# Kernel tuning notes

Measured on AMD Instinct MI355X. Metric: run time of the kernel, lower is better.

## Reference

```python
import jax, jax.numpy as jnp
import numpy as np

D = 768
NH = 12
HD = D // NH
N_MLP = 3072
LN_EPS = 1e-6


def layer_norm(x, g, b, eps=LN_EPS):
    mu = jnp.mean(x, axis=-1, keepdims=True)
    var = jnp.mean(jnp.square(x - mu), axis=-1, keepdims=True)
    return (x - mu) * jax.lax.rsqrt(var + eps) * g + b


def setup_inputs() -> dict:
    key = jax.random.key(0)
    ks = jax.random.split(key, 6)
    x = jax.random.normal(ks[0], (2, 4096, D), dtype=jnp.float32)
    # torch Linear weights are (out, in); init std=0.02, zero bias
    W_qkv = 0.02 * jax.random.normal(ks[1], (3 * D, D), dtype=jnp.float32)
    b_qkv = jnp.zeros((3 * D,), dtype=jnp.float32)
    W_proj = 0.02 * jax.random.normal(ks[2], (D, D), dtype=jnp.float32)
    b_proj = jnp.zeros((D,), dtype=jnp.float32)
    W1 = 0.02 * jax.random.normal(ks[3], (N_MLP, D), dtype=jnp.float32)
    b1 = jnp.zeros((N_MLP,), dtype=jnp.float32)
    W2 = 0.02 * jax.random.normal(ks[4], (D, N_MLP), dtype=jnp.float32)
    b2 = jnp.zeros((D,), dtype=jnp.float32)
    g1 = jnp.ones((D,), dtype=jnp.float32)
    beta1 = jnp.zeros((D,), dtype=jnp.float32)
    g2 = jnp.ones((D,), dtype=jnp.float32)
    beta2 = jnp.zeros((D,), dtype=jnp.float32)
    return dict(x=x, W_qkv=W_qkv, b_qkv=b_qkv, W_proj=W_proj, b_proj=b_proj,
                W1=W1, b1=b1, W2=W2, b2=b2,
                g1=g1, beta1=beta1, g2=g2, beta2=beta2)


def reference(x, W_qkv, b_qkv, W_proj, b_proj, W1, b1, W2, b2, g1, beta1, g2, beta2):
    B, T, d = x.shape
    scale = HD ** (-0.5)
    # --- attention branch (pre-norm) ---
    h = layer_norm(x, g1, beta1)
    qkv = h @ W_qkv.T + b_qkv                      # [B,T,3d]
    qkv = qkv.reshape(B, T, 3, NH, HD)
    q, k, v = qkv[:, :, 0], qkv[:, :, 1], qkv[:, :, 2]  # [B,T,NH,HD]
    logits = jnp.einsum('bthc,bshc->bhts', q, k) * scale
    attn = jax.nn.softmax(logits, axis=-1)
    out = jnp.einsum('bhts,bshc->bthc', attn, v).reshape(B, T, d)
    out = out @ W_proj.T + b_proj
    x = x + out
    # --- MLP branch (pre-norm) ---
    h = layer_norm(x, g2, beta2)
    h = jax.nn.gelu(h @ W1.T + b1, approximate=False)
    h = h @ W2.T + b2
    return x + h
```

## Files before the change

kernel.cpp:

```cpp
#include <hip/hip_runtime.h>
#include <cmath>

typedef __attribute__((ext_vector_type(4))) float f32x4;
typedef __attribute__((ext_vector_type(16))) float f32x16;
typedef __attribute__((ext_vector_type(8))) __bf16 bf16x8;
typedef __attribute__((ext_vector_type(8))) unsigned short u16x8;
typedef __attribute__((ext_vector_type(4))) unsigned short u16x4;
typedef __attribute__((ext_vector_type(2))) unsigned int u32x2;
typedef __attribute__((ext_vector_type(4))) unsigned int u32x4;

#define DEV __device__ __forceinline__

DEV unsigned short f2b(float v) {
  __bf16 b = (__bf16)v;
  return __builtin_bit_cast(unsigned short, b);
}

DEV unsigned int cvtpk(float lo, float hi) {
  unsigned int r;
  asm("v_cvt_pk_bf16_f32 %0, %1, %2" : "=v"(r) : "v"(lo), "v"(hi));
  return r;
}

DEV float exp2a(float x) {
  float r;
  asm("v_exp_f32 %0, %1" : "=v"(r) : "v"(x));
  return r;
}

DEV void swap32(unsigned int& x, unsigned int& y) {
  asm("v_permlane32_swap_b32 %0, %1" : "+v"(x), "+v"(y));
}

DEV u32x2 tr_b16(const unsigned short* p) {
  u32x2 r;
  asm volatile("ds_read_b64_tr_b16 %0, %1"
               : "=v"(r)
               : "v"((unsigned int)(unsigned long long)p)
               : "memory");
  return r;
}

DEV void gll16(const void* g, const void* l) {
  __builtin_amdgcn_global_load_lds(
      (const __attribute__((address_space(1))) unsigned int*)(unsigned long long)g,
      (__attribute__((address_space(3))) unsigned int*)(unsigned int)(unsigned long long)l,
      16, 0, 0);
}

__global__ void k_cvt_bf16(const float* __restrict__ src,
                           unsigned short* __restrict__ dst, int n4) {
  int i = blockIdx.x * blockDim.x + threadIdx.x;
  if (i >= n4) return;
  float4 v = ((const float4*)src)[i];
  u16x4 o = {f2b(v.x), f2b(v.y), f2b(v.z), f2b(v.w)};
  *(u16x4*)(dst + (size_t)i * 4) = o;
}

__global__ void k_ln(const float* __restrict__ x, const float* __restrict__ g,
                     const float* __restrict__ be, unsigned short* __restrict__ out) {
  int row = blockIdx.x;
  int l = threadIdx.x;
  const float* xr = x + (size_t)row * 768;
  float4 v[3];
  float s = 0.f, sq = 0.f;
#pragma unroll
  for (int j = 0; j < 3; ++j) {
    v[j] = ((const float4*)xr)[l + 64 * j];
    s += v[j].x + v[j].y + v[j].z + v[j].w;
    sq += v[j].x * v[j].x + v[j].y * v[j].y + v[j].z * v[j].z + v[j].w * v[j].w;
  }
#pragma unroll
  for (int m = 1; m < 64; m <<= 1) {
    s += __shfl_xor(s, m);
    sq += __shfl_xor(sq, m);
  }
  float mu = s * (1.f / 768.f);
  float var = sq * (1.f / 768.f) - mu * mu;
  float rs = rsqrtf(var + 1e-6f);
  unsigned short* orow = out + (size_t)row * 768;
#pragma unroll
  for (int j = 0; j < 3; ++j) {
    int c4 = l + 64 * j;
    float4 gv = ((const float4*)g)[c4];
    float4 bv = ((const float4*)be)[c4];
    u16x4 o = {f2b((v[j].x - mu) * rs * gv.x + bv.x),
               f2b((v[j].y - mu) * rs * gv.y + bv.y),
               f2b((v[j].z - mu) * rs * gv.z + bv.z),
               f2b((v[j].w - mu) * rs * gv.w + bv.w)};
    *(u16x4*)(orow + c4 * 4) = o;
  }
}

template <int MODE, int BM>
__global__ __launch_bounds__(256) void k_gemm(
    const unsigned short* __restrict__ A, const unsigned short* __restrict__ Bw,
    const float* __restrict__ bias, const float* __restrict__ res,
    void* __restrict__ outp, int N, int K) {
  __shared__ unsigned short As[BM * 32];
  __shared__ unsigned short Bs[128 * 32];
  constexpr int MR = BM / 32;
  constexpr int AI = BM / 64;
  const int tid = threadIdx.x;
  const int w = tid >> 6, l = tid & 63;
  const int wr = w >> 1, wc = w & 1;
  const int lr = l & 15, lg = l >> 4;
  const int nwg = gridDim.x * gridDim.y;
  const int bid = blockIdx.y * gridDim.x + blockIdx.x;
  const int swz = (bid & 7) * (nwg >> 3) + (bid >> 3);
  const int bx = swz % gridDim.x, by = swz / gridDim.x;
  const int brow = by * BM, bcol = bx * 128;
  f32x4 acc[MR][4] = {};
  for (int kt = 0; kt < K; kt += 32) {
    __syncthreads();
#pragma unroll
    for (int i = 0; i < AI; ++i) {
      int c = i * 256 + tid;
      gll16(A + (size_t)(brow + (c >> 2)) * K + kt + (c & 3) * 8,
            (const char*)As + (i * 256 + (w << 6)) * 16);
    }
#pragma unroll
    for (int i = 0; i < 2; ++i) {
      int c = i * 256 + tid;
      gll16(Bw + (size_t)(bcol + (c >> 2)) * K + kt + (c & 3) * 8,
            (const char*)Bs + (i * 256 + (w << 6)) * 16);
    }
    asm volatile("s_waitcnt vmcnt(0)" ::: "memory");
    __syncthreads();
    bf16x8 af[MR], bfr[4];
#pragma unroll
    for (int m = 0; m < MR; ++m)
      af[m] = *(const bf16x8*)&As[(wr * (BM / 2) + m * 16 + lr) * 32 + lg * 8];
#pragma unroll
    for (int n = 0; n < 4; ++n)
      bfr[n] = *(const bf16x8*)&Bs[(wc * 64 + n * 16 + lr) * 32 + lg * 8];
#pragma unroll
    for (int m = 0; m < MR; ++m)
#pragma unroll
      for (int n = 0; n < 4; ++n)
        acc[m][n] = __builtin_amdgcn_mfma_f32_16x16x32_bf16(af[m], bfr[n], acc[m][n], 0, 0, 0);
  }
#pragma unroll
  for (int n = 0; n < 4; ++n) {
    int col = bcol + wc * 64 + n * 16 + lr;
    float bv = bias[col];
#pragma unroll
    for (int m = 0; m < MR; ++m) {
      int row0 = brow + wr * (BM / 2) + m * 16 + lg * 4;
#pragma unroll
      for (int r = 0; r < 4; ++r) {
        size_t idx = (size_t)(row0 + r) * N + col;
        float v = acc[m][n][r] + bv;
        if (MODE == 0) {
          ((unsigned short*)outp)[idx] = f2b(v);
        } else if (MODE == 1) {
          ((float*)outp)[idx] = v + res[idx];
        } else if (MODE == 2) {
          ((unsigned short*)outp)[idx] = f2b(0.5f * v * (1.f + erff(v * 0.70710678f)));
        } else {
          ((float*)outp)[idx] = v + res[idx];
        }
      }
    }
  }
}

__global__ __launch_bounds__(256, 3) void k_attn(const unsigned short* __restrict__ qkv,
                                                 unsigned short* __restrict__ out) {
  __shared__ unsigned short Ks[2][64 * 64];
  __shared__ unsigned short Vs[2][4 * 64 * 16];
  const int tid = threadIdx.x;
  const int w = tid >> 6, l = tid & 63;
  const int lq = l & 31, hi = l >> 5;
  const int p = blockIdx.x;
  const int bid = (p & 7) * 96 + (p >> 3);
  const int bh = bid >> 5, qt = bid & 31;
  const int b = bh / 12, h = bh % 12;
  const size_t base = (size_t)b * 4096 * 2304;
  const int qbase = qt * 128 + w * 32;

  const float SC = 0.18033688f;
  bf16x8 qb[4];
#pragma unroll
  for (int s = 0; s < 4; ++s) {
    u16x8 raw = *(const u16x8*)(qkv + base + (size_t)(qbase + lq) * 2304 + h * 64 +
                                s * 16 + hi * 8);
    u32x4 pk;
#pragma unroll
    for (int d = 0; d < 4; ++d) {
      float f0 = __builtin_bit_cast(float, (unsigned int)raw[2 * d] << 16) * SC;
      float f1 = __builtin_bit_cast(float, (unsigned int)raw[2 * d + 1] << 16) * SC;
      pk[d] = cvtpk(f0, f1);
    }
    qb[s] = __builtin_bit_cast(bf16x8, pk);
  }

  const unsigned short* pK = qkv + base + (size_t)(16 * w + (l >> 3)) * 2304 + 768 +
                             h * 64 + (((l & 7) ^ ((l >> 3) & 7)) << 3);
  const unsigned short* pV =
      qkv + base + (size_t)(l >> 1) * 2304 + 1536 + h * 64 + w * 16 + ((l & 1) << 3);
  const size_t STEP = (size_t)64 * 2304;

  {
    const char* dK = (const char*)&Ks[0][0] + w * 2048;
    const char* dV = (const char*)&Vs[0][0] + w * 2048;
    gll16(pK, dK);
    gll16(pK + 8 * 2304, dK + 1024);
    gll16(pV, dV);
    gll16(pV + 32 * 2304, dV + 1024);
    pK += STEP;
    pV += STEP;
  }

  f32x16 O[2] = {};
  float mrun = -1e30f, lrun = 0.f;

  int it = 0;
  for (int t = 0; t < 64; ++t, it ^= 1) {
    asm volatile("s_waitcnt vmcnt(0)" ::: "memory");
    __syncthreads();
    if (t < 63) {
      const char* dK = (const char*)&Ks[it ^ 1][0] + w * 2048;
      const char* dV = (const char*)&Vs[it ^ 1][0] + w * 2048;
      gll16(pK, dK);
      gll16(pK + 8 * 2304, dK + 1024);
      gll16(pV, dV);
      gll16(pV + 32 * 2304, dV + 1024);
      pK += STEP;
      pV += STEP;
    }

    f32x16 st[2] = {{0}, {0}};
    __builtin_amdgcn_s_setprio(1);
#pragma unroll
    for (int kt = 0; kt < 2; ++kt) {
      int key = kt * 32 + lq;
#pragma unroll
      for (int s = 0; s < 4; ++s) {
        bf16x8 ka =
            *(const bf16x8*)&Ks[it][key * 64 + ((s * 16 + hi * 8) ^ ((key & 7) << 3))];
        st[kt] = __builtin_amdgcn_mfma_f32_32x32x16_bf16(ka, qb[s], st[kt], 0, 0, 0);
      }
    }
    __builtin_amdgcn_s_setprio(0);

    float pmax = st[0][0];
#pragma unroll
    for (int kt = 0; kt < 2; ++kt)
#pragma unroll
      for (int r = (kt == 0 ? 1 : 0); r < 16; ++r) pmax = fmaxf(pmax, st[kt][r]);
    pmax = fmaxf(pmax, __shfl_xor(pmax, 32));
    if (!__all(pmax - mrun <= 11.0f)) {
      float mnew = fmaxf(mrun, pmax);
      float al = exp2a(mrun - mnew);
      lrun *= al;
#pragma unroll
      for (int hb = 0; hb < 2; ++hb)
#pragma unroll
        for (int r = 0; r < 16; ++r) O[hb][r] *= al;
      mrun = mnew;
    }
    float s0 = 0.f;
#pragma unroll
    for (int kt = 0; kt < 2; ++kt)
#pragma unroll
      for (int r = 0; r < 16; ++r) {
        float pv = exp2a(st[kt][r] - mrun);
        st[kt][r] = pv;
        s0 += pv;
      }
    lrun += s0 + __shfl_xor(s0, 32);

    u32x4 pf[4];
#pragma unroll
    for (int kt = 0; kt < 2; ++kt)
#pragma unroll
      for (int h2 = 0; h2 < 2; ++h2) {
        int r0 = h2 * 8;
        unsigned int a0 = cvtpk(st[kt][r0 + 0], st[kt][r0 + 1]);
        unsigned int a1 = cvtpk(st[kt][r0 + 2], st[kt][r0 + 3]);
        unsigned int b0 = cvtpk(st[kt][r0 + 4], st[kt][r0 + 5]);
        unsigned int b1 = cvtpk(st[kt][r0 + 6], st[kt][r0 + 7]);
        swap32(a0, b0);
        swap32(a1, b1);
        pf[kt * 2 + h2] = u32x4{a0, a1, b0, b1};
      }

#pragma unroll
    for (int hb = 0; hb < 2; ++hb) {
      u32x2 vt[4][2];
      const unsigned short* vbase = &Vs[it][(hb * 2 + (lq >> 4)) * 1024 + (lq & 15)];
#pragma unroll
      for (int s = 0; s < 4; ++s)
#pragma unroll
        for (int t2 = 0; t2 < 2; ++t2)
          vt[s][t2] = tr_b16(vbase + ((s * 16 + hi * 8 + t2 * 4) << 4));
      asm volatile("s_waitcnt lgkmcnt(0)" ::: "memory");
      __builtin_amdgcn_sched_barrier(0);
      __builtin_amdgcn_s_setprio(1);
#pragma unroll
      for (int s = 0; s < 4; ++s) {
        u32x4 vv = {vt[s][0].x, vt[s][0].y, vt[s][1].x, vt[s][1].y};
        O[hb] = __builtin_amdgcn_mfma_f32_32x32x16_bf16(
            __builtin_bit_cast(bf16x8, vv), __builtin_bit_cast(bf16x8, pf[s]), O[hb], 0, 0, 0);
      }
      __builtin_amdgcn_s_setprio(0);
    }
  }

  float rl = 1.f / lrun;
  unsigned short* orow = out + (size_t)(b * 4096 + qbase + lq) * 768 + h * 64;
#pragma unroll
  for (int hb = 0; hb < 2; ++hb)
#pragma unroll
    for (int g = 0; g < 4; ++g) {
      unsigned int d0 = cvtpk(O[hb][4 * g + 0] * rl, O[hb][4 * g + 1] * rl);
      unsigned int d1 = cvtpk(O[hb][4 * g + 2] * rl, O[hb][4 * g + 3] * rl);
      *(u32x2*)(orow + hb * 32 + 8 * g + 4 * hi) = u32x2{d0, d1};
    }
}

extern "C" void kernel_launch(void* const* d_in, const int* in_sizes, int n_in,
                              void* d_out, int out_size, void* d_ws, size_t ws_size,
                              hipStream_t stream) {
  const float* x = (const float*)d_in[0];
  const float* Wqkv = (const float*)d_in[1];
  const float* bqkv = (const float*)d_in[2];
  const float* Wproj = (const float*)d_in[3];
  const float* bproj = (const float*)d_in[4];
  const float* W1 = (const float*)d_in[5];
  const float* b1 = (const float*)d_in[6];
  const float* W2 = (const float*)d_in[7];
  const float* b2 = (const float*)d_in[8];
  const float* g1 = (const float*)d_in[9];
  const float* be1 = (const float*)d_in[10];
  const float* g2 = (const float*)d_in[11];
  const float* be2 = (const float*)d_in[12];

  char* ws = (char*)d_ws;
  unsigned short* wqkv = (unsigned short*)(ws + 0);
  unsigned short* wproj = (unsigned short*)(ws + 3538944);
  unsigned short* ww1 = (unsigned short*)(ws + 4718592);
  unsigned short* ww2 = (unsigned short*)(ws + 9437184);
  unsigned short* h1 = (unsigned short*)(ws + 14155776);
  unsigned short* qkvb = (unsigned short*)(ws + 26738688);
  unsigned short* attno = (unsigned short*)(ws + 64487424);
  float* x1 = (float*)(ws + 77070336);
  unsigned short* h2 = (unsigned short*)(ws + 102236160);
  unsigned short* m1 = (unsigned short*)(ws + 114819072);

  k_cvt_bf16<<<1728, 256, 0, stream>>>(Wqkv, wqkv, 442368);
  k_cvt_bf16<<<576, 256, 0, stream>>>(Wproj, wproj, 147456);
  k_cvt_bf16<<<2304, 256, 0, stream>>>(W1, ww1, 589824);
  k_cvt_bf16<<<2304, 256, 0, stream>>>(W2, ww2, 589824);

  k_ln<<<8192, 64, 0, stream>>>(x, g1, be1, h1);
  k_gemm<0, 128><<<dim3(18, 64), 256, 0, stream>>>(h1, wqkv, bqkv, nullptr, qkvb, 2304, 768);
  k_attn<<<768, 256, 0, stream>>>(qkvb, attno);
  k_gemm<1, 64><<<dim3(6, 128), 256, 0, stream>>>(attno, wproj, bproj, x, x1, 768, 768);
  k_ln<<<8192, 64, 0, stream>>>(x1, g2, be2, h2);
  k_gemm<2, 128><<<dim3(24, 64), 256, 0, stream>>>(h2, ww1, b1, nullptr, m1, 3072, 768);
  k_gemm<3, 64><<<dim3(6, 128), 256, 0, stream>>>(m1, ww2, b2, x1, (float*)d_out, 768, 3072);
}
```

Baseline: 374.4 us.

## Split attention KV into two halves with merge kernel; widen GEMM K-tile with swizzled LDS

Attention now splits each query tile's 4096-key range into two 2048-key halves. That doubles the grid to 1536 workgroups and raises the occupancy hint to 4. Partial unnormalised outputs and running max/sum are written to fp32 scratch, reusing the m1 and h1 buffers, and a new merge kernel combines them with rescaling. Separately, the GEMM K-step goes from 32 to 64, with an XOR-swizzled LDS layout to avoid bank conflicts, which halves the barrier and wait count per K. The costs are extra global traffic for the fp32 partials, an extra launch, and larger LDS use per GEMM block.

Result: faster. 365.6 us (-2.3%).

```diff
diff --git a/kernel.cpp b/kernel.cpp
--- a/kernel.cpp
+++ b/kernel.cpp
@@ -97,10 +97,10 @@
     const unsigned short* __restrict__ A, const unsigned short* __restrict__ Bw,
     const float* __restrict__ bias, const float* __restrict__ res,
     void* __restrict__ outp, int N, int K) {
-  __shared__ unsigned short As[BM * 32];
-  __shared__ unsigned short Bs[128 * 32];
+  __shared__ unsigned short As[BM * 64];
+  __shared__ unsigned short Bs[128 * 64];
   constexpr int MR = BM / 32;
-  constexpr int AI = BM / 64;
+  constexpr int AI = BM / 32;
   const int tid = threadIdx.x;
   const int w = tid >> 6, l = tid & 63;
   const int wr = w >> 1, wc = w & 1;
@@ -111,34 +111,47 @@
   const int bx = swz % gridDim.x, by = swz / gridDim.x;
   const int brow = by * BM, bcol = bx * 128;
   f32x4 acc[MR][4] = {};
-  for (int kt = 0; kt < K; kt += 32) {
+  for (int kt = 0; kt < K; kt += 64) {
     __syncthreads();
 #pragma unroll
     for (int i = 0; i < AI; ++i) {
       int c = i * 256 + tid;
-      gll16(A + (size_t)(brow + (c >> 2)) * K + kt + (c & 3) * 8,
+      int row = c >> 3, cg = (c & 7) ^ (row & 7);
+      gll16(A + (size_t)(brow + row) * K + kt + cg * 8,
             (const char*)As + (i * 256 + (w << 6)) * 16);
     }
 #pragma unroll
-    for (int i = 0; i < 2; ++i) {
+    for (int i = 0; i < 4; ++i) {
       int c = i * 256 + tid;
-      gll16(Bw + (size_t)(bcol + (c >> 2)) * K + kt + (c & 3) * 8,
+      int row = c >> 3, cg = (c & 7) ^ (row & 7);
+      gll16(Bw + (size_t)(bcol + row) * K + kt + cg * 8,
             (const char*)Bs + (i * 256 + (w << 6)) * 16);
     }
     asm volatile("s_waitcnt vmcnt(0)" ::: "memory");
     __syncthreads();
-    bf16x8 af[MR], bfr[4];
-#pragma unroll
-    for (int m = 0; m < MR; ++m)
-      af[m] = *(const bf16x8*)&As[(wr * (BM / 2) + m * 16 + lr) * 32 + lg * 8];
-#pragma unroll
-    for (int n = 0; n < 4; ++n)
-      bfr[n] = *(const bf16x8*)&Bs[(wc * 64 + n * 16 + lr) * 32 + lg * 8];
-#pragma unroll
-    for (int m = 0; m < MR; ++m)
-#pragma unroll
-      for (int n = 0; n < 4; ++n)
-        acc[m][n] = __builtin_amdgcn_mfma_f32_16x16x32_bf16(af[m], bfr[n], acc[m][n], 0, 0, 0);
+    bf16x8 af[MR][2], bfr[4][2];
+#pragma unroll
+    for (int m = 0; m < MR; ++m) {
+      int row = wr * (BM / 2) + m * 16 + lr;
+#pragma unroll
+      for (int s = 0; s < 2; ++s)
+        af[m][s] = *(const bf16x8*)&As[row * 64 + (((s * 4 + lg) ^ (row & 7)) << 3)];
+    }
+#pragma unroll
+    for (int n = 0; n < 4; ++n) {
+      int row = wc * 64 + n * 16 + lr;
+#pragma unroll
+      for (int s = 0; s < 2; ++s)
+        bfr[n][s] = *(const bf16x8*)&Bs[row * 64 + (((s * 4 + lg) ^ (row & 7)) << 3)];
+    }
+#pragma unroll
+    for (int s = 0; s < 2; ++s)
+#pragma unroll
+      for (int m = 0; m < MR; ++m)
+#pragma unroll
+        for (int n = 0; n < 4; ++n)
+          acc[m][n] =
+              __builtin_amdgcn_mfma_f32_16x16x32_bf16(af[m][s], bfr[n][s], acc[m][n], 0, 0, 0);
   }
 #pragma unroll
   for (int n = 0; n < 4; ++n) {
@@ -165,19 +178,22 @@
   }
 }
 
-__global__ __launch_bounds__(256, 3) void k_attn(const unsigned short* __restrict__ qkv,
-                                                 unsigned short* __restrict__ out) {
+__global__ __launch_bounds__(256, 4) void k_attn(const unsigned short* __restrict__ qkv,
+                                                 f32x4* __restrict__ Opart,
+                                                 float* __restrict__ ml) {
   __shared__ unsigned short Ks[2][64 * 64];
   __shared__ unsigned short Vs[2][4 * 64 * 16];
   const int tid = threadIdx.x;
   const int w = tid >> 6, l = tid & 63;
   const int lq = l & 31, hi = l >> 5;
   const int p = blockIdx.x;
-  const int bid = (p & 7) * 96 + (p >> 3);
-  const int bh = bid >> 5, qt = bid & 31;
+  const int linear = (p & 7) * 192 + (p >> 3);
+  const int bh = linear >> 6, rem = linear & 63;
+  const int qt = rem >> 1, half = rem & 1;
   const int b = bh / 12, h = bh % 12;
   const size_t base = (size_t)b * 4096 * 2304;
   const int qbase = qt * 128 + w * 32;
+  const int kv0 = half * 2048;
 
   const float SC = 0.18033688f;
   bf16x8 qb[4];
@@ -195,10 +211,10 @@
     qb[s] = __builtin_bit_cast(bf16x8, pk);
   }
 
-  const unsigned short* pK = qkv + base + (size_t)(16 * w + (l >> 3)) * 2304 + 768 +
+  const unsigned short* pK = qkv + base + (size_t)(kv0 + 16 * w + (l >> 3)) * 2304 + 768 +
                              h * 64 + (((l & 7) ^ ((l >> 3) & 7)) << 3);
-  const unsigned short* pV =
-      qkv + base + (size_t)(l >> 1) * 2304 + 1536 + h * 64 + w * 16 + ((l & 1) << 3);
+  const unsigned short* pV = qkv + base + (size_t)(kv0 + (l >> 1)) * 2304 + 1536 + h * 64 +
+                             w * 16 + ((l & 1) << 3);
   const size_t STEP = (size_t)64 * 2304;
 
   {
@@ -216,10 +232,10 @@
   float mrun = -1e30f, lrun = 0.f;
 
   int it = 0;
-  for (int t = 0; t < 64; ++t, it ^= 1) {
+  for (int t = 0; t < 32; ++t, it ^= 1) {
     asm volatile("s_waitcnt vmcnt(0)" ::: "memory");
     __syncthreads();
-    if (t < 63) {
+    if (t < 31) {
       const char* dK = (const char*)&Ks[it ^ 1][0] + w * 2048;
       const char* dV = (const char*)&Vs[it ^ 1][0] + w * 2048;
       gll16(pK, dK);
@@ -308,15 +324,52 @@
     }
   }
 
-  float rl = 1.f / lrun;
-  unsigned short* orow = out + (size_t)(b * 4096 + qbase + lq) * 768 + h * 64;
+  if (hi == 0) {
+    ml[((linear * 4 + w) * 2 + 0) * 32 + lq] = mrun;
+    ml[((linear * 4 + w) * 2 + 1) * 32 + lq] = lrun;
+  }
 #pragma unroll
   for (int hb = 0; hb < 2; ++hb)
 #pragma unroll
     for (int g = 0; g < 4; ++g) {
-      unsigned int d0 = cvtpk(O[hb][4 * g + 0] * rl, O[hb][4 * g + 1] * rl);
-      unsigned int d1 = cvtpk(O[hb][4 * g + 2] * rl, O[hb][4 * g + 3] * rl);
-      *(u32x2*)(orow + hb * 32 + 8 * g + 4 * hi) = u32x2{d0, d1};
+      int k = hb * 4 + g;
+      f32x4 v = {O[hb][4 * g + 0], O[hb][4 * g + 1], O[hb][4 * g + 2], O[hb][4 * g + 3]};
+      Opart[((linear * 4 + w) * 8 + k) * 64 + l] = v;
+    }
+}
+
+__global__ __launch_bounds__(256) void k_merge(const f32x4* __restrict__ Opart,
+                                               const float* __restrict__ ml,
+                                               unsigned short* __restrict__ out) {
+  const int g = blockIdx.x;
+  const int bh = g >> 5, qt = g & 31;
+  const int b = bh / 12, h = bh % 12;
+  const int tid = threadIdx.x;
+  const int w = tid >> 6, l = tid & 63;
+  const int lq = l & 31, hi = l >> 5;
+  const int bidA = bh * 64 + qt * 2;
+  const int bidB = bidA + 1;
+  float m0 = ml[((bidA * 4 + w) * 2 + 0) * 32 + lq];
+  float l0 = ml[((bidA * 4 + w) * 2 + 1) * 32 + lq];
+  float m1 = ml[((bidB * 4 + w) * 2 + 0) * 32 + lq];
+  float l1 = ml[((bidB * 4 + w) * 2 + 1) * 32 + lq];
+  float m = fmaxf(m0, m1);
+  float w0 = exp2a(m0 - m), w1 = exp2a(m1 - m);
+  float rl = 1.f / (l0 * w0 + l1 * w1);
+  float a0 = w0 * rl, a1 = w1 * rl;
+  const int t = qt * 128 + w * 32 + lq;
+  unsigned short* orow = out + (size_t)(b * 4096 + t) * 768 + h * 64;
+#pragma unroll
+  for (int hb = 0; hb < 2; ++hb)
+#pragma unroll
+    for (int gg = 0; gg < 4; ++gg) {
+      int k = hb * 4 + gg;
+      f32x4 va = Opart[((bidA * 4 + w) * 8 + k) * 64 + l];
+      f32x4 vb = Opart[((bidB * 4 + w) * 8 + k) * 64 + l];
+      f32x4 v = va * a0 + vb * a1;
+      unsigned int d0 = cvtpk(v[0], v[1]);
+      unsigned int d1 = cvtpk(v[2], v[3]);
+      *(u32x2*)(orow + hb * 32 + 8 * gg + 4 * hi) = u32x2{d0, d1};
     }
 }
 
@@ -348,6 +401,8 @@
   float* x1 = (float*)(ws + 77070336);
   unsigned short* h2 = (unsigned short*)(ws + 102236160);
   unsigned short* m1 = (unsigned short*)(ws + 114819072);
+  f32x4* Opart = (f32x4*)m1;
+  float* mlbuf = (float*)h1;
 
   k_cvt_bf16<<<1728, 256, 0, stream>>>(Wqkv, wqkv, 442368);
   k_cvt_bf16<<<576, 256, 0, stream>>>(Wproj, wproj, 147456);
@@ -356,7 +411,8 @@
 
   k_ln<<<8192, 64, 0, stream>>>(x, g1, be1, h1);
   k_gemm<0, 128><<<dim3(18, 64), 256, 0, stream>>>(h1, wqkv, bqkv, nullptr, qkvb, 2304, 768);
-  k_attn<<<768, 256, 0, stream>>>(qkvb, attno);
+  k_attn<<<1536, 256, 0, stream>>>(qkvb, Opart, mlbuf);
+  k_merge<<<768, 256, 0, stream>>>(Opart, mlbuf, attno);
   k_gemm<1, 64><<<dim3(6, 128), 256, 0, stream>>>(attno, wproj, bproj, x, x1, 768, 768);
   k_ln<<<8192, 64, 0, stream>>>(x1, g2, be2, h2);
   k_gemm<2, 128><<<dim3(24, 64), 256, 0, stream>>>(h2, ww1, b1, nullptr, m1, 3072, 768);
```
